# Kernel tuning notes

Measured on AMD Instinct MI355X. Metric: run time of the kernel, lower is better.

The kernel has to match this reference:

```python
import jax, jax.numpy as jnp
import numpy as np

BATCH, DIM = 8192, 1024  # batch of ODE states, state dimension (orig dim=100 scaled up)
ETA = 1.0                # self.eta
B_DECAY = 1.0            # self.B (linear decay coefficient)


def setup_inputs() -> dict:
    key = jax.random.key(0)
    k1, k2, k3, k4, k5 = jax.random.split(key, 5)
    return {
        "x":      jax.random.normal(k1, (BATCH, DIM), jnp.float32),
        "e_x":    jax.random.normal(k2, (BATCH, DIM), jnp.float32),
        "W":      jax.random.normal(k3, (BATCH, DIM), jnp.float32),
        "A":      jax.random.normal(k4, (DIM, DIM), jnpp := jnp.float32) / np.float32(np.sqrt(DIM)),
        "target": jax.random.normal(k5, (1, DIM), jnp.float32),
    }


def reference(x, e_x, W, A, target):
    # b_ast = diagonal of B_ast = diag(target^2 / (1 + target^2)); mm with a diag
    # matrix == elementwise multiply by its diagonal.  [1, D]
    b_ast = target ** 2 / (1.0 + target ** 2)
    # control: u = -eta * (W * (x + e_x - target)) @ B_ast              [B, D]
    u = -ETA * (W * ((x + e_x) - target)) * b_ast
    # saturating nonlinearity sigma(x) = x^2 / (1 + x^2)                [B, D]
    sig = x ** 2 / (1.0 + x ** 2)
    # dx = -B*x + A @ sigma(x) (per state: sigma(x) @ A^T) + u*sigma(x) [B, D]
    dx = -B_DECAY * x + sig @ A.T + u * sig
    # original returns tuple(dx_i) + tuple(-dx_i) + tuple(zeros): stack as [3, B, D]
    return jnp.stack([dx, -dx, jnp.zeros_like(dx)])
```

## Files before the change

kernel.cpp:

```cpp
#include <hip/hip_runtime.h>
#include <hip/hip_bf16.h>
#include <stdint.h>

#define BATCH 8192
#define DIM   1024
#define BM 64
#define BN 64
#define BK 64
#define NT (DIM / BK)

typedef __attribute__((ext_vector_type(4))) float f32x4;
typedef __attribute__((ext_vector_type(8))) short bf16x8;
typedef __attribute__((ext_vector_type(4))) unsigned short u16x4;
typedef __attribute__((ext_vector_type(8))) unsigned short u16x8;

#define AS1(p) ((const __attribute__((address_space(1))) void*)(p))
#define AS3(p) ((__attribute__((address_space(3))) void*)(p))

__device__ __forceinline__ unsigned short f2bf(float f) {
    union { __hip_bfloat16 h; unsigned short u; } v;
    v.h = __hip_bfloat16(f);
    return v.u;
}

__device__ __forceinline__ float sigma_f(float x) {
    float x2 = x * x;
    return x2 * __builtin_amdgcn_rcpf(1.0f + x2);
}

__global__ __launch_bounds__(256) void convA_kernel(
    const float* __restrict__ A, unsigned short* __restrict__ Ab)
{
    int idx = blockIdx.x * 256 + threadIdx.x;
    f32x4 av = ((const f32x4*)A)[idx];
    u16x4 ab;
#pragma unroll
    for (int i = 0; i < 4; ++i) ab[i] = f2bf(av[i]);
    ((u16x4*)Ab)[idx] = ab;
}

__global__ __launch_bounds__(256, 5) void fused_kernel(
    const float* __restrict__ x, const float* __restrict__ ex,
    const float* __restrict__ W, const float* __restrict__ tgt,
    const unsigned short* __restrict__ Ab,
    float* __restrict__ out0, float* __restrict__ out1,
    float* __restrict__ out2)
{
    __shared__ __align__(16) char lds[32768];

    const int b     = blockIdx.x;
    const int xcd   = b & 7;
    const int local = b >> 3;
    const int bm    = xcd * 16 + (local >> 4);
    const int bn    = local & 15;

    const int tid  = threadIdx.x;
    const int lane = tid & 63;
    const int wid  = tid >> 6;
    const int wr   = wid >> 1;
    const int wc   = wid & 1;
    const int l15  = lane & 15;

    const int swz = (((lane & 7) ^ (lane >> 3)) << 4);
    const char* gBb = (const char*)Ab +
        ((size_t)(bn * BN + wid * 16 + (lane >> 3)) * DIM) * 2 + swz;

    const int r0 = tid >> 3;
    const int g  = tid & 7;
    const float* gx = x + (size_t)(bm * BM + r0) * DIM + g * 8;
    const int wAoff = (g * 16) ^ ((r0 & 7) << 4);

    const int rd_sw = (lane & 7) << 4;
    const int cb0   = (lane >> 4) << 4;

    f32x4 acc[2][2];
#pragma unroll
    for (int mi = 0; mi < 2; ++mi)
#pragma unroll
        for (int ni = 0; ni < 2; ++ni)
            acc[mi][ni] = f32x4{0.f, 0.f, 0.f, 0.f};

    auto stageB = [&](int k, char* Bs) {
#pragma unroll
        for (int j = 0; j < 2; ++j)
            __builtin_amdgcn_global_load_lds(
                AS1(gBb + (size_t)j * (8 * DIM * 2) + (size_t)k * 2),
                AS3(Bs + (wid * 16 + j * 8) * 128), 16, 0, 0);
    };
    auto loadX = [&](int k, f32x4 xa[2][2]) {
#pragma unroll
        for (int s = 0; s < 2; ++s) {
            xa[s][0] = *(const f32x4*)(gx + (size_t)s * 32 * DIM + k);
            xa[s][1] = *(const f32x4*)(gx + (size_t)s * 32 * DIM + k + 4);
        }
    };
    auto writeSig = [&](char* As, f32x4 xa[2][2]) {
#pragma unroll
        for (int s = 0; s < 2; ++s) {
            u16x8 sb;
#pragma unroll
            for (int i = 0; i < 4; ++i) {
                sb[i]     = f2bf(sigma_f(xa[s][0][i]));
                sb[i + 4] = f2bf(sigma_f(xa[s][1][i]));
            }
            *(u16x8*)(As + (r0 + s * 32) * 128 + wAoff) = sb;
        }
    };

    {
        f32x4 xa[2][2];
        loadX(0, xa);
        stageB(0, lds + 8192);
        writeSig(lds, xa);
    }
    __syncthreads();

    for (int t = 0; t < NT; ++t) {
        const int cur = t & 1;
        f32x4 xa[2][2];
        if (t + 1 < NT) {
            loadX((t + 1) * BK, xa);
            stageB((t + 1) * BK, lds + (cur ^ 1) * 16384 + 8192);
        }
        __builtin_amdgcn_sched_barrier(0);

        const char* As_ = lds + cur * 16384;
        const char* Bs_ = As_ + 8192;
#pragma unroll
        for (int kk = 0; kk < 2; ++kk) {
            bf16x8 af[2], bfr[2];
#pragma unroll
            for (int mi = 0; mi < 2; ++mi)
                af[mi] = *(const bf16x8*)(As_ + (wr * 32 + mi * 16 + l15) * 128 +
                                          ((cb0 + kk * 64) ^ rd_sw));
#pragma unroll
            for (int ni = 0; ni < 2; ++ni)
                bfr[ni] = *(const bf16x8*)(Bs_ + (wc * 32 + ni * 16 + l15) * 128 +
                                           ((cb0 + kk * 64) ^ rd_sw));
#pragma unroll
            for (int mi = 0; mi < 2; ++mi)
#pragma unroll
                for (int ni = 0; ni < 2; ++ni)
                    acc[mi][ni] = __builtin_amdgcn_mfma_f32_16x16x32_bf16(
                        af[mi], bfr[ni], acc[mi][ni], 0, 0, 0);
        }
        __builtin_amdgcn_sched_barrier(0);

        if (t + 1 < NT) writeSig(lds + (cur ^ 1) * 16384, xa);
        __syncthreads();
    }

#pragma unroll
    for (int mi = 0; mi < 2; ++mi)
#pragma unroll
        for (int ni = 0; ni < 2; ++ni) {
            const int row_ = wr * 32 + mi * 16 + ((lane >> 4) << 2);
            const int colb = (wc * 32 + ni * 16 + l15) * 4;
#pragma unroll
            for (int r = 0; r < 4; ++r)
                *(float*)(lds + (row_ + r) * 256 + colb) = acc[mi][ni][r];
        }
    __syncthreads();

#pragma unroll
    for (int p = 0; p < 4; ++p) {
        const int ci  = tid + p * 256;
        const int row = ci >> 4;
        const int cv  = ci & 15;
        f32x4 c = *(const f32x4*)(lds + row * 256 + cv * 16);
        const size_t v4 = (size_t)(bm * BM + row) * (DIM / 4) + bn * (BN / 4) + cv;
        f32x4 xv = ((const f32x4*)x)[v4];
        f32x4 ev = ((const f32x4*)ex)[v4];
        f32x4 wv = ((const f32x4*)W)[v4];
        f32x4 tv = ((const f32x4*)tgt)[bn * (BN / 4) + cv];
        f32x4 o0;
#pragma unroll
        for (int e = 0; e < 4; ++e) {
            float xi = xv[e], ti = tv[e];
            float ba = ti * ti * __builtin_amdgcn_rcpf(1.0f + ti * ti);
            float u  = -(wv[e] * (xi + ev[e] - ti)) * ba;
            float s  = sigma_f(xi);
            o0[e] = -xi + u * s + c[e];
        }
        ((f32x4*)out0)[v4] = o0;
        ((f32x4*)out1)[v4] = -o0;
        ((f32x4*)out2)[v4] = f32x4{0.f, 0.f, 0.f, 0.f};
    }
}

extern "C" void kernel_launch(void* const* d_in, const int* in_sizes, int n_in,
                              void* d_out, int out_size, void* d_ws, size_t ws_size,
                              hipStream_t stream)
{
    const float* x   = (const float*)d_in[0];
    const float* ex  = (const float*)d_in[1];
    const float* W   = (const float*)d_in[2];
    const float* A   = (const float*)d_in[3];
    const float* tgt = (const float*)d_in[4];

    float* out0 = (float*)d_out;
    float* out1 = out0 + (size_t)BATCH * DIM;
    float* out2 = out1 + (size_t)BATCH * DIM;

    unsigned short* Abf = (unsigned short*)d_ws;

    convA_kernel<<<DIM * DIM / 4 / 256, 256, 0, stream>>>(A, Abf);
    fused_kernel<<<(BATCH / BM) * (DIM / BN), 256, 0, stream>>>(
        x, ex, W, tgt, Abf, out0, out1, out2);
}
```

Baseline: 65.63 us.

## Load GEMM operands directly into registers and enlarge tile to 128x64

The main GEMM loop no longer stages sigma(x) and bf16 A tiles through shared memory. Each wave now loads its own x rows and the B fragments from global memory straight into MFMA operand layout, computes sigma in registers, and double-buffers these register sets without any __syncthreads. The block tile grows to 128x64 with one wave per 32-row strip, and the XCD block mapping is changed. This removes LDS traffic and barriers, but every wave reloads the full B tile, which increases global/L2 traffic, and register pressure rises (launch bounds drop from 5 to 4).

```diff
diff --git a/kernel.cpp b/kernel.cpp
--- a/kernel.cpp
+++ b/kernel.cpp
@@ -4,18 +4,11 @@
 
 #define BATCH 8192
 #define DIM   1024
-#define BM 64
-#define BN 64
-#define BK 64
-#define NT (DIM / BK)
 
 typedef __attribute__((ext_vector_type(4))) float f32x4;
 typedef __attribute__((ext_vector_type(8))) short bf16x8;
 typedef __attribute__((ext_vector_type(4))) unsigned short u16x4;
 typedef __attribute__((ext_vector_type(8))) unsigned short u16x8;
-
-#define AS1(p) ((const __attribute__((address_space(1))) void*)(p))
-#define AS3(p) ((__attribute__((address_space(3))) void*)(p))
 
 __device__ __forceinline__ unsigned short f2bf(float f) {
     union { __hip_bfloat16 h; unsigned short u; } v;
@@ -39,7 +32,7 @@
     ((u16x4*)Ab)[idx] = ab;
 }
 
-__global__ __launch_bounds__(256, 5) void fused_kernel(
+__global__ __launch_bounds__(256, 4) void fused_kernel(
     const float* __restrict__ x, const float* __restrict__ ex,
     const float* __restrict__ W, const float* __restrict__ tgt,
     const unsigned short* __restrict__ Ab,
@@ -48,114 +41,79 @@
 {
     __shared__ __align__(16) char lds[32768];
 
-    const int b     = blockIdx.x;
-    const int xcd   = b & 7;
-    const int local = b >> 3;
-    const int bm    = xcd * 16 + (local >> 4);
-    const int bn    = local & 15;
+    const int b    = blockIdx.x;
+    const int xcd  = b & 7;
+    const int idx  = b >> 3;
+    const int bm   = (idx >> 4) * 8 + xcd;
+    const int bn   = idx & 15;
 
     const int tid  = threadIdx.x;
     const int lane = tid & 63;
     const int wid  = tid >> 6;
-    const int wr   = wid >> 1;
-    const int wc   = wid & 1;
     const int l15  = lane & 15;
+    const int kgo  = (lane >> 4) << 3;
 
-    const int swz = (((lane & 7) ^ (lane >> 3)) << 4);
-    const char* gBb = (const char*)Ab +
-        ((size_t)(bn * BN + wid * 16 + (lane >> 3)) * DIM) * 2 + swz;
+    const float* gxa0 = x + (size_t)(bm * 128 + wid * 32 + l15) * DIM + kgo;
+    const float* gxa1 = gxa0 + (size_t)16 * DIM;
+    const unsigned short* gb0 = Ab + (size_t)(bn * 64 + l15) * DIM + kgo;
 
-    const int r0 = tid >> 3;
-    const int g  = tid & 7;
-    const float* gx = x + (size_t)(bm * BM + r0) * DIM + g * 8;
-    const int wAoff = (g * 16) ^ ((r0 & 7) << 4);
-
-    const int rd_sw = (lane & 7) << 4;
-    const int cb0   = (lane >> 4) << 4;
-
-    f32x4 acc[2][2];
+    f32x4 acc[2][4];
 #pragma unroll
     for (int mi = 0; mi < 2; ++mi)
 #pragma unroll
-        for (int ni = 0; ni < 2; ++ni)
+        for (int ni = 0; ni < 4; ++ni)
             acc[mi][ni] = f32x4{0.f, 0.f, 0.f, 0.f};
 
-    auto stageB = [&](int k, char* Bs) {
+    f32x4 xe[2][2], xo[2][2];
+    bf16x8 be[4], bo[4];
+
+    auto LOADX = [&](int kt, f32x4 xa[2][2]) {
+        xa[0][0] = *(const f32x4*)(gxa0 + kt * 32);
+        xa[0][1] = *(const f32x4*)(gxa0 + kt * 32 + 4);
+        xa[1][0] = *(const f32x4*)(gxa1 + kt * 32);
+        xa[1][1] = *(const f32x4*)(gxa1 + kt * 32 + 4);
+    };
+    auto LOADB = [&](int kt, bf16x8 bf[4]) {
 #pragma unroll
-        for (int j = 0; j < 2; ++j)
-            __builtin_amdgcn_global_load_lds(
-                AS1(gBb + (size_t)j * (8 * DIM * 2) + (size_t)k * 2),
-                AS3(Bs + (wid * 16 + j * 8) * 128), 16, 0, 0);
+        for (int ni = 0; ni < 4; ++ni)
+            bf[ni] = *(const bf16x8*)(gb0 + (size_t)ni * 16 * DIM + kt * 32);
     };
-    auto loadX = [&](int k, f32x4 xa[2][2]) {
+    auto COMPUTE = [&](f32x4 xa[2][2], bf16x8 bf[4]) {
 #pragma unroll
-        for (int s = 0; s < 2; ++s) {
-            xa[s][0] = *(const f32x4*)(gx + (size_t)s * 32 * DIM + k);
-            xa[s][1] = *(const f32x4*)(gx + (size_t)s * 32 * DIM + k + 4);
-        }
-    };
-    auto writeSig = [&](char* As, f32x4 xa[2][2]) {
-#pragma unroll
-        for (int s = 0; s < 2; ++s) {
-            u16x8 sb;
+        for (int mi = 0; mi < 2; ++mi) {
+            union { u16x8 u; bf16x8 b; } cv;
 #pragma unroll
             for (int i = 0; i < 4; ++i) {
-                sb[i]     = f2bf(sigma_f(xa[s][0][i]));
-                sb[i + 4] = f2bf(sigma_f(xa[s][1][i]));
+                cv.u[i]     = f2bf(sigma_f(xa[mi][0][i]));
+                cv.u[i + 4] = f2bf(sigma_f(xa[mi][1][i]));
             }
-            *(u16x8*)(As + (r0 + s * 32) * 128 + wAoff) = sb;
+#pragma unroll
+            for (int ni = 0; ni < 4; ++ni)
+                acc[mi][ni] = __builtin_amdgcn_mfma_f32_16x16x32_bf16(
+                    cv.b, bf[ni], acc[mi][ni], 0, 0, 0);
         }
     };
 
-    {
-        f32x4 xa[2][2];
-        loadX(0, xa);
-        stageB(0, lds + 8192);
-        writeSig(lds, xa);
-    }
-    __syncthreads();
-
-    for (int t = 0; t < NT; ++t) {
-        const int cur = t & 1;
-        f32x4 xa[2][2];
-        if (t + 1 < NT) {
-            loadX((t + 1) * BK, xa);
-            stageB((t + 1) * BK, lds + (cur ^ 1) * 16384 + 8192);
-        }
+    LOADX(0, xe);
+    LOADB(0, be);
+#pragma unroll
+    for (int kt = 0; kt < 32; kt += 2) {
+        if (kt + 1 < 32) { LOADX(kt + 1, xo); LOADB(kt + 1, bo); }
         __builtin_amdgcn_sched_barrier(0);
-
-        const char* As_ = lds + cur * 16384;
-        const char* Bs_ = As_ + 8192;
-#pragma unroll
-        for (int kk = 0; kk < 2; ++kk) {
-            bf16x8 af[2], bfr[2];
-#pragma unroll
-            for (int mi = 0; mi < 2; ++mi)
-                af[mi] = *(const bf16x8*)(As_ + (wr * 32 + mi * 16 + l15) * 128 +
-                                          ((cb0 + kk * 64) ^ rd_sw));
-#pragma unroll
-            for (int ni = 0; ni < 2; ++ni)
-                bfr[ni] = *(const bf16x8*)(Bs_ + (wc * 32 + ni * 16 + l15) * 128 +
-                                           ((cb0 + kk * 64) ^ rd_sw));
-#pragma unroll
-            for (int mi = 0; mi < 2; ++mi)
-#pragma unroll
-                for (int ni = 0; ni < 2; ++ni)
-                    acc[mi][ni] = __builtin_amdgcn_mfma_f32_16x16x32_bf16(
-                        af[mi], bfr[ni], acc[mi][ni], 0, 0, 0);
-        }
+        COMPUTE(xe, be);
         __builtin_amdgcn_sched_barrier(0);
-
-        if (t + 1 < NT) writeSig(lds + (cur ^ 1) * 16384, xa);
-        __syncthreads();
+        if (kt + 2 < 32) { LOADX(kt + 2, xe); LOADB(kt + 2, be); }
+        __builtin_amdgcn_sched_barrier(0);
+        COMPUTE(xo, bo);
+        __builtin_amdgcn_sched_barrier(0);
     }
 
 #pragma unroll
     for (int mi = 0; mi < 2; ++mi)
 #pragma unroll
-        for (int ni = 0; ni < 2; ++ni) {
-            const int row_ = wr * 32 + mi * 16 + ((lane >> 4) << 2);
-            const int colb = (wc * 32 + ni * 16 + l15) * 4;
+        for (int ni = 0; ni < 4; ++ni) {
+            const int row_ = wid * 32 + mi * 16 + ((lane >> 4) << 2);
+            const int colb = (ni * 16 + l15) * 4;
 #pragma unroll
             for (int r = 0; r < 4; ++r)
                 *(float*)(lds + (row_ + r) * 256 + colb) = acc[mi][ni][r];
@@ -163,16 +121,16 @@
     __syncthreads();
 
 #pragma unroll
-    for (int p = 0; p < 4; ++p) {
+    for (int p = 0; p < 8; ++p) {
         const int ci  = tid + p * 256;
         const int row = ci >> 4;
         const int cv  = ci & 15;
         f32x4 c = *(const f32x4*)(lds + row * 256 + cv * 16);
-        const size_t v4 = (size_t)(bm * BM + row) * (DIM / 4) + bn * (BN / 4) + cv;
+        const size_t v4 = (size_t)(bm * 128 + row) * (DIM / 4) + bn * 16 + cv;
         f32x4 xv = ((const f32x4*)x)[v4];
         f32x4 ev = ((const f32x4*)ex)[v4];
         f32x4 wv = ((const f32x4*)W)[v4];
-        f32x4 tv = ((const f32x4*)tgt)[bn * (BN / 4) + cv];
+        f32x4 tv = ((const f32x4*)tgt)[bn * 16 + cv];
         f32x4 o0;
 #pragma unroll
         for (int e = 0; e < 4; ++e) {
@@ -205,6 +163,6 @@
     unsigned short* Abf = (unsigned short*)d_ws;
 
     convA_kernel<<<DIM * DIM / 4 / 256, 256, 0, stream>>>(A, Abf);
-    fused_kernel<<<(BATCH / BM) * (DIM / BN), 256, 0, stream>>>(
+    fused_kernel<<<(BATCH / 128) * (DIM / 64), 256, 0, stream>>>(
         x, ex, W, tgt, Abf, out0, out1, out2);
 }
```

New measurement: 134.5 us. 2.05x slower.

## Persistent two-tile blocks with queued decoupled epilogue via bf16 C workspace

Applied to the files above, without the earlier changes.

Switches to a persistent grid of 512 blocks. Each block computes two 128x64 GEMM tiles and writes each result as bf16 into a global workspace. A global atomic queue then hands finished tiles to any block, which runs the elementwise epilogue, and zero-filling of out2 is spread between the phases. The aim is to overlap the memory-bound epilogue stores with the MFMA work and get larger tile reuse. In exchange it adds a spin-wait queue, an extra bf16 round trip for C that costs precision, and it needs the 512 blocks to be co-resident to avoid deadlock.

```diff
diff --git a/kernel.cpp b/kernel.cpp
--- a/kernel.cpp
+++ b/kernel.cpp
@@ -4,10 +4,11 @@
 
 #define BATCH 8192
 #define DIM   1024
-#define BM 64
+#define BM 128
 #define BN 64
 #define BK 64
-#define NT (DIM / BK)
+#define NT 16
+#define NTILE 1024
 
 typedef __attribute__((ext_vector_type(4))) float f32x4;
 typedef __attribute__((ext_vector_type(8))) short bf16x8;
@@ -22,16 +23,21 @@
     v.h = __hip_bfloat16(f);
     return v.u;
 }
-
+__device__ __forceinline__ float bf2f(unsigned short u) {
+    union { unsigned int i; float f; } v; v.i = (unsigned int)u << 16;
+    return v.f;
+}
 __device__ __forceinline__ float sigma_f(float x) {
     float x2 = x * x;
     return x2 * __builtin_amdgcn_rcpf(1.0f + x2);
 }
 
 __global__ __launch_bounds__(256) void convA_kernel(
-    const float* __restrict__ A, unsigned short* __restrict__ Ab)
+    const float* __restrict__ A, unsigned short* __restrict__ Ab,
+    unsigned* __restrict__ hdr)
 {
     int idx = blockIdx.x * 256 + threadIdx.x;
+    if (idx < 2 + NTILE) hdr[idx] = 0;
     f32x4 av = ((const f32x4*)A)[idx];
     u16x4 ab;
 #pragma unroll
@@ -39,152 +45,213 @@
     ((u16x4*)Ab)[idx] = ab;
 }
 
-__global__ __launch_bounds__(256, 5) void fused_kernel(
+__global__ __launch_bounds__(256, 2) void fused_kernel(
     const float* __restrict__ x, const float* __restrict__ ex,
     const float* __restrict__ W, const float* __restrict__ tgt,
     const unsigned short* __restrict__ Ab,
+    unsigned short* __restrict__ Cws, unsigned* __restrict__ hdr,
     float* __restrict__ out0, float* __restrict__ out1,
     float* __restrict__ out2)
 {
-    __shared__ __align__(16) char lds[32768];
-
-    const int b     = blockIdx.x;
-    const int xcd   = b & 7;
-    const int local = b >> 3;
-    const int bm    = xcd * 16 + (local >> 4);
-    const int bn    = local & 15;
+    __shared__ __align__(16) char lds[81920];
+    __shared__ int shE;
+    char* Cl = lds + 49152;
+
+    const int b   = blockIdx.x;
+    const int bsw = (b & 7) * 64 + (b >> 3);
+    const int T0  = bsw, T1 = bsw + 512;
 
     const int tid  = threadIdx.x;
     const int lane = tid & 63;
     const int wid  = tid >> 6;
-    const int wr   = wid >> 1;
-    const int wc   = wid & 1;
+    const int wr   = wid >> 1, wc = wid & 1;
     const int l15  = lane & 15;
-
-    const int swz = (((lane & 7) ^ (lane >> 3)) << 4);
-    const char* gBb = (const char*)Ab +
-        ((size_t)(bn * BN + wid * 16 + (lane >> 3)) * DIM) * 2 + swz;
-
-    const int r0 = tid >> 3;
-    const int g  = tid & 7;
-    const float* gx = x + (size_t)(bm * BM + r0) * DIM + g * 8;
+    const int swz  = (((lane & 7) ^ (lane >> 3)) << 4);
+    const int r0   = tid >> 3;
+    const int g    = tid & 7;
     const int wAoff = (g * 16) ^ ((r0 & 7) << 4);
-
     const int rd_sw = (lane & 7) << 4;
     const int cb0   = (lane >> 4) << 4;
 
-    f32x4 acc[2][2];
-#pragma unroll
-    for (int mi = 0; mi < 2; ++mi)
-#pragma unroll
-        for (int ni = 0; ni < 2; ++ni)
-            acc[mi][ni] = f32x4{0.f, 0.f, 0.f, 0.f};
-
-    auto stageB = [&](int k, char* Bs) {
-#pragma unroll
-        for (int j = 0; j < 2; ++j)
-            __builtin_amdgcn_global_load_lds(
-                AS1(gBb + (size_t)j * (8 * DIM * 2) + (size_t)k * 2),
-                AS3(Bs + (wid * 16 + j * 8) * 128), 16, 0, 0);
-    };
-    auto loadX = [&](int k, f32x4 xa[2][2]) {
-#pragma unroll
-        for (int s = 0; s < 2; ++s) {
-            xa[s][0] = *(const f32x4*)(gx + (size_t)s * 32 * DIM + k);
-            xa[s][1] = *(const f32x4*)(gx + (size_t)s * 32 * DIM + k + 4);
-        }
-    };
-    auto writeSig = [&](char* As, f32x4 xa[2][2]) {
-#pragma unroll
-        for (int s = 0; s < 2; ++s) {
-            u16x8 sb;
-#pragma unroll
-            for (int i = 0; i < 4; ++i) {
-                sb[i]     = f2bf(sigma_f(xa[s][0][i]));
-                sb[i + 4] = f2bf(sigma_f(xa[s][1][i]));
-            }
-            *(u16x8*)(As + (r0 + s * 32) * 128 + wAoff) = sb;
-        }
-    };
-
-    {
-        f32x4 xa[2][2];
-        loadX(0, xa);
-        stageB(0, lds + 8192);
-        writeSig(lds, xa);
-    }
-    __syncthreads();
-
-    for (int t = 0; t < NT; ++t) {
-        const int cur = t & 1;
-        f32x4 xa[2][2];
-        if (t + 1 < NT) {
-            loadX((t + 1) * BK, xa);
-            stageB((t + 1) * BK, lds + (cur ^ 1) * 16384 + 8192);
-        }
-        __builtin_amdgcn_sched_barrier(0);
-
-        const char* As_ = lds + cur * 16384;
-        const char* Bs_ = As_ + 8192;
-#pragma unroll
-        for (int kk = 0; kk < 2; ++kk) {
-            bf16x8 af[2], bfr[2];
-#pragma unroll
-            for (int mi = 0; mi < 2; ++mi)
-                af[mi] = *(const bf16x8*)(As_ + (wr * 32 + mi * 16 + l15) * 128 +
-                                          ((cb0 + kk * 64) ^ rd_sw));
+    unsigned* q = hdr + 2;
+
+    auto gemmTile = [&](int t) {
+        const int bm = t >> 4, bn = t & 15;
+        const float* gx = x + (size_t)(bm * BM + r0) * DIM + g * 8;
+        const char* gBb = (const char*)Ab +
+            ((size_t)(bn * BN + wid * 8 + (lane >> 3)) * DIM) * 2 + swz;
+
+        f32x4 acc[4][2];
+#pragma unroll
+        for (int mi = 0; mi < 4; ++mi)
 #pragma unroll
             for (int ni = 0; ni < 2; ++ni)
-                bfr[ni] = *(const bf16x8*)(Bs_ + (wc * 32 + ni * 16 + l15) * 128 +
-                                           ((cb0 + kk * 64) ^ rd_sw));
-#pragma unroll
-            for (int mi = 0; mi < 2; ++mi)
+                acc[mi][ni] = f32x4{0.f, 0.f, 0.f, 0.f};
+
+        auto stageB = [&](int k, char* Bs) {
+#pragma unroll
+            for (int j = 0; j < 2; ++j)
+                __builtin_amdgcn_global_load_lds(
+                    AS1(gBb + (size_t)j * (32 * DIM * 2) + (size_t)k * 2),
+                    AS3(Bs + (wid * 8 + j * 32) * 128), 16, 0, 0);
+        };
+        auto loadX = [&](int k, f32x4 xa[4][2]) {
+#pragma unroll
+            for (int s = 0; s < 4; ++s) {
+                xa[s][0] = *(const f32x4*)(gx + (size_t)s * 32 * DIM + k);
+                xa[s][1] = *(const f32x4*)(gx + (size_t)s * 32 * DIM + k + 4);
+            }
+        };
+        auto writeSig = [&](char* As, f32x4 xa[4][2]) {
+#pragma unroll
+            for (int s = 0; s < 4; ++s) {
+                u16x8 sb;
+#pragma unroll
+                for (int i = 0; i < 4; ++i) {
+                    sb[i]     = f2bf(sigma_f(xa[s][0][i]));
+                    sb[i + 4] = f2bf(sigma_f(xa[s][1][i]));
+                }
+                *(u16x8*)(As + (r0 + s * 32) * 128 + wAoff) = sb;
+            }
+        };
+
+        {
+            f32x4 xa[4][2];
+            loadX(0, xa);
+            stageB(0, lds + 16384);
+            writeSig(lds, xa);
+        }
+        __syncthreads();
+
+        for (int it = 0; it < NT; ++it) {
+            const int cur = it & 1;
+            char* bufn = lds + (cur ^ 1) * 24576;
+            f32x4 xa[4][2];
+            if (it + 1 < NT) {
+                loadX((it + 1) * BK, xa);
+                stageB((it + 1) * BK, bufn + 16384);
+            }
+            __builtin_amdgcn_sched_barrier(0);
+            const char* As_ = lds + cur * 24576;
+            const char* Bs_ = As_ + 16384;
+#pragma unroll
+            for (int kk = 0; kk < 2; ++kk) {
+                bf16x8 af[4], bfr[2];
+#pragma unroll
+                for (int mi = 0; mi < 4; ++mi)
+                    af[mi] = *(const bf16x8*)(As_ + (wr * 64 + mi * 16 + l15) * 128 +
+                                              ((cb0 + kk * 64) ^ rd_sw));
 #pragma unroll
                 for (int ni = 0; ni < 2; ++ni)
-                    acc[mi][ni] = __builtin_amdgcn_mfma_f32_16x16x32_bf16(
-                        af[mi], bfr[ni], acc[mi][ni], 0, 0, 0);
-        }
-        __builtin_amdgcn_sched_barrier(0);
-
-        if (t + 1 < NT) writeSig(lds + (cur ^ 1) * 16384, xa);
-        __syncthreads();
-    }
-
-#pragma unroll
-    for (int mi = 0; mi < 2; ++mi)
-#pragma unroll
-        for (int ni = 0; ni < 2; ++ni) {
-            const int row_ = wr * 32 + mi * 16 + ((lane >> 4) << 2);
-            const int colb = (wc * 32 + ni * 16 + l15) * 4;
-#pragma unroll
-            for (int r = 0; r < 4; ++r)
-                *(float*)(lds + (row_ + r) * 256 + colb) = acc[mi][ni][r];
-        }
-    __syncthreads();
-
-#pragma unroll
-    for (int p = 0; p < 4; ++p) {
-        const int ci  = tid + p * 256;
-        const int row = ci >> 4;
-        const int cv  = ci & 15;
-        f32x4 c = *(const f32x4*)(lds + row * 256 + cv * 16);
-        const size_t v4 = (size_t)(bm * BM + row) * (DIM / 4) + bn * (BN / 4) + cv;
-        f32x4 xv = ((const f32x4*)x)[v4];
-        f32x4 ev = ((const f32x4*)ex)[v4];
-        f32x4 wv = ((const f32x4*)W)[v4];
-        f32x4 tv = ((const f32x4*)tgt)[bn * (BN / 4) + cv];
-        f32x4 o0;
-#pragma unroll
-        for (int e = 0; e < 4; ++e) {
-            float xi = xv[e], ti = tv[e];
-            float ba = ti * ti * __builtin_amdgcn_rcpf(1.0f + ti * ti);
-            float u  = -(wv[e] * (xi + ev[e] - ti)) * ba;
-            float s  = sigma_f(xi);
-            o0[e] = -xi + u * s + c[e];
-        }
-        ((f32x4*)out0)[v4] = o0;
-        ((f32x4*)out1)[v4] = -o0;
-        ((f32x4*)out2)[v4] = f32x4{0.f, 0.f, 0.f, 0.f};
+                    bfr[ni] = *(const bf16x8*)(Bs_ + (wc * 32 + ni * 16 + l15) * 128 +
+                                               ((cb0 + kk * 64) ^ rd_sw));
+#pragma unroll
+                for (int mi = 0; mi < 4; ++mi)
+#pragma unroll
+                    for (int ni = 0; ni < 2; ++ni)
+                        acc[mi][ni] = __builtin_amdgcn_mfma_f32_16x16x32_bf16(
+                            af[mi], bfr[ni], acc[mi][ni], 0, 0, 0);
+            }
+            __builtin_amdgcn_sched_barrier(0);
+            if (it + 1 < NT) writeSig(bufn, xa);
+            __syncthreads();
+        }
+
+#pragma unroll
+        for (int mi = 0; mi < 4; ++mi)
+#pragma unroll
+            for (int ni = 0; ni < 2; ++ni) {
+                const int row_ = wr * 64 + mi * 16 + ((lane >> 4) << 2);
+                const int colb = (wc * 32 + ni * 16 + l15) * 4;
+#pragma unroll
+                for (int r = 0; r < 4; ++r)
+                    *(float*)(Cl + (row_ + r) * 256 + colb) = acc[mi][ni][r];
+            }
+        __syncthreads();
+
+        u16x4* Cq = (u16x4*)Cws + (size_t)t * 2048;
+#pragma unroll
+        for (int p = 0; p < 8; ++p) {
+            const int ci = p * 256 + tid, row = ci >> 4, cv = ci & 15;
+            f32x4 c = *(const f32x4*)(Cl + row * 256 + cv * 16);
+            u16x4 cb;
+#pragma unroll
+            for (int e = 0; e < 4; ++e) cb[e] = f2bf(c[e]);
+            Cq[ci] = cb;
+        }
+        __syncthreads();
+    };
+
+    auto pushT = [&](int t) {
+        if (tid == 0) {
+            unsigned slot = atomicAdd(&hdr[0], 1u);
+            __hip_atomic_store(&q[slot], (unsigned)(t + 1),
+                               __ATOMIC_RELEASE, __HIP_MEMORY_SCOPE_AGENT);
+        }
+    };
+
+    auto popEpi = [&]() {
+        if (tid == 0) {
+            unsigned tk = atomicAdd(&hdr[1], 1u);
+            unsigned v;
+            for (;;) {
+                v = __hip_atomic_load(&q[tk], __ATOMIC_RELAXED,
+                                      __HIP_MEMORY_SCOPE_AGENT);
+                if (v) break;
+                __builtin_amdgcn_s_sleep(2);
+            }
+            (void)__hip_atomic_load(&q[tk], __ATOMIC_ACQUIRE,
+                                    __HIP_MEMORY_SCOPE_AGENT);
+            shE = (int)v - 1;
+        }
+        __syncthreads();
+        const int e   = shE;
+        const int ebm = e >> 4, ebn = e & 15;
+        const u16x4* Cq = (const u16x4*)Cws + (size_t)e * 2048;
+#pragma unroll
+        for (int p = 0; p < 8; ++p) {
+            const int ci = p * 256 + tid, row = ci >> 4, cv = ci & 15;
+            u16x4 cb = Cq[ci];
+            const size_t v4 = (size_t)(ebm * BM + row) * (DIM / 4) + ebn * 16 + cv;
+            f32x4 xv = ((const f32x4*)x)[v4];
+            f32x4 evv = ((const f32x4*)ex)[v4];
+            f32x4 wv = ((const f32x4*)W)[v4];
+            f32x4 tv = ((const f32x4*)tgt)[ebn * 16 + cv];
+            f32x4 o0;
+#pragma unroll
+            for (int ee = 0; ee < 4; ++ee) {
+                float xi = xv[ee], ti = tv[ee];
+                float ba = ti * ti * __builtin_amdgcn_rcpf(1.0f + ti * ti);
+                float u  = -(wv[ee] * (xi + evv[ee] - ti)) * ba;
+                float s  = sigma_f(xi);
+                o0[ee] = -xi + u * s + bf2f(cb[ee]);
+            }
+            ((f32x4*)out0)[v4] = o0;
+            ((f32x4*)out1)[v4] = -o0;
+        }
+        __syncthreads();
+    };
+
+    auto zeroT = [&](int t) {
+        const int zbm = t >> 4, zbn = t & 15;
+#pragma unroll
+        for (int p = 0; p < 8; ++p) {
+            const int ci = p * 256 + tid, row = ci >> 4, cv = ci & 15;
+            ((f32x4*)out2)[(size_t)(zbm * BM + row) * (DIM / 4) + zbn * 16 + cv] =
+                f32x4{0.f, 0.f, 0.f, 0.f};
+        }
+    };
+
+    gemmTile(T0); pushT(T0);
+    if (b & 1) {
+        popEpi();
+        zeroT(T0); zeroT(T1);
+        gemmTile(T1); pushT(T1);
+        popEpi();
+    } else {
+        gemmTile(T1); pushT(T1);
+        zeroT(T0); zeroT(T1);
+        popEpi(); popEpi();
     }
 }
 
@@ -203,8 +270,10 @@
     float* out2 = out1 + (size_t)BATCH * DIM;
 
     unsigned short* Abf = (unsigned short*)d_ws;
-
-    convA_kernel<<<DIM * DIM / 4 / 256, 256, 0, stream>>>(A, Abf);
-    fused_kernel<<<(BATCH / BM) * (DIM / BN), 256, 0, stream>>>(
-        x, ex, W, tgt, Abf, out0, out1, out2);
-}
+    unsigned short* Cws = (unsigned short*)((char*)d_ws + (size_t)2 * 1024 * 1024);
+    unsigned*       hdr = (unsigned*)((char*)d_ws + (size_t)18 * 1024 * 1024);
+
+    convA_kernel<<<DIM * DIM / 4 / 256, 256, 0, stream>>>(A, Abf, hdr);
+    fused_kernel<<<512, 256, 0, stream>>>(x, ex, W, tgt, Abf, Cws, hdr,
+                                          out0, out1, out2);
+}
```

Result: slower. 147.4 us (+124.6%).

## Split work into concurrent GEMM and elementwise blocks plus bf16 combine pass

Applied to the files above, without the earlier changes.

The separate A-to-bf16 conversion kernel is removed; A is now converted to bf16 while it is staged into LDS. The first kernel interleaves GEMM blocks (128x64 tiles) with elementwise blocks that compute the bias term and the zero output, so memory-bound and MFMA work can overlap. The GEMM result goes to a bf16 workspace, and a second kernel adds it to out0 and writes out1. The cost is extra round trips: out0 is written and read back, the workspace is written and read, and the GEMM result picks up additional bf16 rounding.

```diff
diff --git a/kernel.cpp b/kernel.cpp
--- a/kernel.cpp
+++ b/kernel.cpp
@@ -4,187 +4,216 @@
 
 #define BATCH 8192
 #define DIM   1024
-#define BM 64
+#define BM 128
 #define BN 64
 #define BK 64
-#define NT (DIM / BK)
+#define NT 16
+#define NV4 (BATCH * DIM / 4)
 
 typedef __attribute__((ext_vector_type(4))) float f32x4;
 typedef __attribute__((ext_vector_type(8))) short bf16x8;
 typedef __attribute__((ext_vector_type(4))) unsigned short u16x4;
 typedef __attribute__((ext_vector_type(8))) unsigned short u16x8;
 
-#define AS1(p) ((const __attribute__((address_space(1))) void*)(p))
-#define AS3(p) ((__attribute__((address_space(3))) void*)(p))
-
 __device__ __forceinline__ unsigned short f2bf(float f) {
     union { __hip_bfloat16 h; unsigned short u; } v;
     v.h = __hip_bfloat16(f);
     return v.u;
 }
-
+__device__ __forceinline__ float bf2f(unsigned short u) {
+    union { unsigned int i; float f; } v; v.i = (unsigned int)u << 16;
+    return v.f;
+}
 __device__ __forceinline__ float sigma_f(float x) {
     float x2 = x * x;
     return x2 * __builtin_amdgcn_rcpf(1.0f + x2);
 }
 
-__global__ __launch_bounds__(256) void convA_kernel(
-    const float* __restrict__ A, unsigned short* __restrict__ Ab)
-{
-    int idx = blockIdx.x * 256 + threadIdx.x;
-    f32x4 av = ((const f32x4*)A)[idx];
-    u16x4 ab;
-#pragma unroll
-    for (int i = 0; i < 4; ++i) ab[i] = f2bf(av[i]);
-    ((u16x4*)Ab)[idx] = ab;
-}
-
-__global__ __launch_bounds__(256, 5) void fused_kernel(
+__global__ __launch_bounds__(256, 3) void k1_kernel(
     const float* __restrict__ x, const float* __restrict__ ex,
     const float* __restrict__ W, const float* __restrict__ tgt,
-    const unsigned short* __restrict__ Ab,
-    float* __restrict__ out0, float* __restrict__ out1,
-    float* __restrict__ out2)
+    const float* __restrict__ A,
+    unsigned short* __restrict__ Cws,
+    float* __restrict__ out0, float* __restrict__ out2)
 {
-    __shared__ __align__(16) char lds[32768];
-
-    const int b     = blockIdx.x;
-    const int xcd   = b & 7;
-    const int local = b >> 3;
-    const int bm    = xcd * 16 + (local >> 4);
-    const int bn    = local & 15;
-
-    const int tid  = threadIdx.x;
-    const int lane = tid & 63;
-    const int wid  = tid >> 6;
-    const int wr   = wid >> 1;
-    const int wc   = wid & 1;
-    const int l15  = lane & 15;
-
-    const int swz = (((lane & 7) ^ (lane >> 3)) << 4);
-    const char* gBb = (const char*)Ab +
-        ((size_t)(bn * BN + wid * 16 + (lane >> 3)) * DIM) * 2 + swz;
-
-    const int r0 = tid >> 3;
-    const int g  = tid & 7;
-    const float* gx = x + (size_t)(bm * BM + r0) * DIM + g * 8;
-    const int wAoff = (g * 16) ^ ((r0 & 7) << 4);
-
-    const int rd_sw = (lane & 7) << 4;
-    const int cb0   = (lane >> 4) << 4;
-
-    f32x4 acc[2][2];
-#pragma unroll
-    for (int mi = 0; mi < 2; ++mi)
-#pragma unroll
-        for (int ni = 0; ni < 2; ++ni)
-            acc[mi][ni] = f32x4{0.f, 0.f, 0.f, 0.f};
-
-    auto stageB = [&](int k, char* Bs) {
-#pragma unroll
-        for (int j = 0; j < 2; ++j)
-            __builtin_amdgcn_global_load_lds(
-                AS1(gBb + (size_t)j * (8 * DIM * 2) + (size_t)k * 2),
-                AS3(Bs + (wid * 16 + j * 8) * 128), 16, 0, 0);
-    };
-    auto loadX = [&](int k, f32x4 xa[2][2]) {
-#pragma unroll
-        for (int s = 0; s < 2; ++s) {
-            xa[s][0] = *(const f32x4*)(gx + (size_t)s * 32 * DIM + k);
-            xa[s][1] = *(const f32x4*)(gx + (size_t)s * 32 * DIM + k + 4);
+    __shared__ __align__(16) char lds[49152];
+
+    const int b = blockIdx.x;
+    const int tid = threadIdx.x;
+
+    if (((b >> 3) & 1) == 0) {
+        const int gt = (b >> 4) * 8 + (b & 7);
+        const int bm = gt >> 4;
+        const int bn = gt & 15;
+
+        const int lane = tid & 63;
+        const int wid  = tid >> 6;
+        const int wr   = wid >> 1, wc = wid & 1;
+        const int l15  = lane & 15;
+        const int r0   = tid >> 3;
+        const int g    = tid & 7;
+        const int wAoff = (g * 16) ^ ((r0 & 7) << 4);
+        const int rd_sw = (lane & 7) << 4;
+        const int cb0   = (lane >> 4) << 4;
+
+        const float* gx = x + (size_t)(bm * BM + r0) * DIM + g * 8;
+        const float* gA = A + (size_t)(bn * BN + r0) * DIM + g * 8;
+
+        f32x4 acc[4][2];
+#pragma unroll
+        for (int mi = 0; mi < 4; ++mi)
+#pragma unroll
+            for (int ni = 0; ni < 2; ++ni)
+                acc[mi][ni] = f32x4{0.f, 0.f, 0.f, 0.f};
+
+        f32x4 xa[4][2], bv[2][2];
+
+        auto loadX = [&](int k) {
+#pragma unroll
+            for (int s = 0; s < 4; ++s) {
+                xa[s][0] = *(const f32x4*)(gx + (size_t)s * 32 * DIM + k);
+                xa[s][1] = *(const f32x4*)(gx + (size_t)s * 32 * DIM + k + 4);
+            }
+        };
+        auto loadB = [&](int k) {
+#pragma unroll
+            for (int s = 0; s < 2; ++s) {
+                bv[s][0] = *(const f32x4*)(gA + (size_t)s * 32 * DIM + k);
+                bv[s][1] = *(const f32x4*)(gA + (size_t)s * 32 * DIM + k + 4);
+            }
+        };
+        auto writeStage = [&](char* buf) {
+            char* As = buf;
+            char* Bs = buf + 16384;
+#pragma unroll
+            for (int s = 0; s < 4; ++s) {
+                u16x8 sb;
+#pragma unroll
+                for (int i = 0; i < 4; ++i) {
+                    sb[i]     = f2bf(sigma_f(xa[s][0][i]));
+                    sb[i + 4] = f2bf(sigma_f(xa[s][1][i]));
+                }
+                *(u16x8*)(As + (r0 + s * 32) * 128 + wAoff) = sb;
+            }
+#pragma unroll
+            for (int s = 0; s < 2; ++s) {
+                u16x8 sb;
+#pragma unroll
+                for (int i = 0; i < 4; ++i) {
+                    sb[i]     = f2bf(bv[s][0][i]);
+                    sb[i + 4] = f2bf(bv[s][1][i]);
+                }
+                *(u16x8*)(Bs + (r0 + s * 32) * 128 + wAoff) = sb;
+            }
+        };
+
+        loadX(0); loadB(0);
+        writeStage(lds);
+        __syncthreads();
+
+        for (int t = 0; t < NT; ++t) {
+            const int cur = t & 1;
+            if (t + 1 < NT) { loadX((t + 1) * BK); loadB((t + 1) * BK); }
+            __builtin_amdgcn_sched_barrier(0);
+
+            const char* As_ = lds + cur * 24576;
+            const char* Bs_ = As_ + 16384;
+#pragma unroll
+            for (int kk = 0; kk < 2; ++kk) {
+                bf16x8 af[4], bfr[2];
+#pragma unroll
+                for (int mi = 0; mi < 4; ++mi)
+                    af[mi] = *(const bf16x8*)(As_ + (wr * 64 + mi * 16 + l15) * 128 +
+                                              ((cb0 + kk * 64) ^ rd_sw));
+#pragma unroll
+                for (int ni = 0; ni < 2; ++ni)
+                    bfr[ni] = *(const bf16x8*)(Bs_ + (wc * 32 + ni * 16 + l15) * 128 +
+                                               ((cb0 + kk * 64) ^ rd_sw));
+#pragma unroll
+                for (int mi = 0; mi < 4; ++mi)
+#pragma unroll
+                    for (int ni = 0; ni < 2; ++ni)
+                        acc[mi][ni] = __builtin_amdgcn_mfma_f32_16x16x32_bf16(
+                            af[mi], bfr[ni], acc[mi][ni], 0, 0, 0);
+            }
+            __builtin_amdgcn_sched_barrier(0);
+            if (t + 1 < NT) writeStage(lds + (cur ^ 1) * 24576);
+            __syncthreads();
         }
-    };
-    auto writeSig = [&](char* As, f32x4 xa[2][2]) {
-#pragma unroll
-        for (int s = 0; s < 2; ++s) {
-            u16x8 sb;
-#pragma unroll
-            for (int i = 0; i < 4; ++i) {
-                sb[i]     = f2bf(sigma_f(xa[s][0][i]));
-                sb[i + 4] = f2bf(sigma_f(xa[s][1][i]));
-            }
-            *(u16x8*)(As + (r0 + s * 32) * 128 + wAoff) = sb;
+
+#pragma unroll
+        for (int mi = 0; mi < 4; ++mi)
+#pragma unroll
+            for (int ni = 0; ni < 2; ++ni) {
+                const int row_ = wr * 64 + mi * 16 + ((lane >> 4) << 2);
+                const int colb = (wc * 32 + ni * 16 + l15) * 4;
+#pragma unroll
+                for (int r = 0; r < 4; ++r)
+                    *(float*)(lds + (row_ + r) * 256 + colb) = acc[mi][ni][r];
+            }
+        __syncthreads();
+
+        unsigned short* Ct = Cws + (size_t)gt * (BM * BN);
+#pragma unroll
+        for (int p = 0; p < 4; ++p) {
+            const int ci  = p * 256 + tid;
+            const int row = ci >> 3;
+            const int gg  = ci & 7;
+            f32x4 c0 = *(const f32x4*)(lds + row * 256 + gg * 32);
+            f32x4 c1 = *(const f32x4*)(lds + row * 256 + gg * 32 + 16);
+            u16x8 cb;
+#pragma unroll
+            for (int e = 0; e < 4; ++e) {
+                cb[e]     = f2bf(c0[e]);
+                cb[e + 4] = f2bf(c1[e]);
+            }
+            *(u16x8*)(Ct + row * BN + gg * 8) = cb;
         }
-    };
-
-    {
-        f32x4 xa[2][2];
-        loadX(0, xa);
-        stageB(0, lds + 8192);
-        writeSig(lds, xa);
+    } else {
+        const int s = (b >> 4) * 8 + (b & 7);
+        const int i0 = s * 256 + tid;
+#pragma unroll
+        for (int p = 0; p < 8; ++p) {
+            const int v4 = i0 + p * 262144;
+            const int cv = v4 & 255;
+            f32x4 xv = ((const f32x4*)x)[v4];
+            f32x4 ev = ((const f32x4*)ex)[v4];
+            f32x4 wv = ((const f32x4*)W)[v4];
+            f32x4 tv = ((const f32x4*)tgt)[cv];
+            f32x4 bq;
+#pragma unroll
+            for (int e = 0; e < 4; ++e) {
+                float xi = xv[e], ti = tv[e];
+                float ba = ti * ti * __builtin_amdgcn_rcpf(1.0f + ti * ti);
+                float u  = -(wv[e] * (xi + ev[e] - ti)) * ba;
+                float sg = sigma_f(xi);
+                bq[e] = -xi + u * sg;
+            }
+            ((f32x4*)out0)[v4] = bq;
+            ((f32x4*)out2)[v4] = f32x4{0.f, 0.f, 0.f, 0.f};
+        }
     }
-    __syncthreads();
-
-    for (int t = 0; t < NT; ++t) {
-        const int cur = t & 1;
-        f32x4 xa[2][2];
-        if (t + 1 < NT) {
-            loadX((t + 1) * BK, xa);
-            stageB((t + 1) * BK, lds + (cur ^ 1) * 16384 + 8192);
-        }
-        __builtin_amdgcn_sched_barrier(0);
-
-        const char* As_ = lds + cur * 16384;
-        const char* Bs_ = As_ + 8192;
-#pragma unroll
-        for (int kk = 0; kk < 2; ++kk) {
-            bf16x8 af[2], bfr[2];
-#pragma unroll
-            for (int mi = 0; mi < 2; ++mi)
-                af[mi] = *(const bf16x8*)(As_ + (wr * 32 + mi * 16 + l15) * 128 +
-                                          ((cb0 + kk * 64) ^ rd_sw));
-#pragma unroll
-            for (int ni = 0; ni < 2; ++ni)
-                bfr[ni] = *(const bf16x8*)(Bs_ + (wc * 32 + ni * 16 + l15) * 128 +
-                                           ((cb0 + kk * 64) ^ rd_sw));
-#pragma unroll
-            for (int mi = 0; mi < 2; ++mi)
-#pragma unroll
-                for (int ni = 0; ni < 2; ++ni)
-                    acc[mi][ni] = __builtin_amdgcn_mfma_f32_16x16x32_bf16(
-                        af[mi], bfr[ni], acc[mi][ni], 0, 0, 0);
-        }
-        __builtin_amdgcn_sched_barrier(0);
-
-        if (t + 1 < NT) writeSig(lds + (cur ^ 1) * 16384, xa);
-        __syncthreads();
-    }
-
-#pragma unroll
-    for (int mi = 0; mi < 2; ++mi)
-#pragma unroll
-        for (int ni = 0; ni < 2; ++ni) {
-            const int row_ = wr * 32 + mi * 16 + ((lane >> 4) << 2);
-            const int colb = (wc * 32 + ni * 16 + l15) * 4;
-#pragma unroll
-            for (int r = 0; r < 4; ++r)
-                *(float*)(lds + (row_ + r) * 256 + colb) = acc[mi][ni][r];
-        }
-    __syncthreads();
-
+}
+
+__global__ __launch_bounds__(256) void k2_kernel(
+    const unsigned short* __restrict__ Cws,
+    float* __restrict__ out0, float* __restrict__ out1)
+{
+    const int i0 = blockIdx.x * 256 + threadIdx.x;
 #pragma unroll
     for (int p = 0; p < 4; ++p) {
-        const int ci  = tid + p * 256;
-        const int row = ci >> 4;
-        const int cv  = ci & 15;
-        f32x4 c = *(const f32x4*)(lds + row * 256 + cv * 16);
-        const size_t v4 = (size_t)(bm * BM + row) * (DIM / 4) + bn * (BN / 4) + cv;
-        f32x4 xv = ((const f32x4*)x)[v4];
-        f32x4 ev = ((const f32x4*)ex)[v4];
-        f32x4 wv = ((const f32x4*)W)[v4];
-        f32x4 tv = ((const f32x4*)tgt)[bn * (BN / 4) + cv];
+        const int v4  = i0 + p * 524288;
+        const int m   = v4 >> 8;
+        const int cv  = v4 & 255;
+        const int gt  = (m >> 7) * 16 + (cv >> 4);
+        const int off = (m & 127) * BN + (cv & 15) * 4;
+        u16x4 cb = *(const u16x4*)(Cws + (size_t)gt * (BM * BN) + off);
+        f32x4 bq = ((const f32x4*)out0)[v4];
         f32x4 o0;
 #pragma unroll
-        for (int e = 0; e < 4; ++e) {
-            float xi = xv[e], ti = tv[e];
-            float ba = ti * ti * __builtin_amdgcn_rcpf(1.0f + ti * ti);
-            float u  = -(wv[e] * (xi + ev[e] - ti)) * ba;
-            float s  = sigma_f(xi);
-            o0[e] = -xi + u * s + c[e];
-        }
+        for (int e = 0; e < 4; ++e) o0[e] = bq[e] + bf2f(cb[e]);
         ((f32x4*)out0)[v4] = o0;
         ((f32x4*)out1)[v4] = -o0;
-        ((f32x4*)out2)[v4] = f32x4{0.f, 0.f, 0.f, 0.f};
     }
 }
 
@@ -202,9 +231,8 @@
     float* out1 = out0 + (size_t)BATCH * DIM;
     float* out2 = out1 + (size_t)BATCH * DIM;
 
-    unsigned short* Abf = (unsigned short*)d_ws;
-
-    convA_kernel<<<DIM * DIM / 4 / 256, 256, 0, stream>>>(A, Abf);
-    fused_kernel<<<(BATCH / BM) * (DIM / BN), 256, 0, stream>>>(
-        x, ex, W, tgt, Abf, out0, out1, out2);
-}
+    unsigned short* Cws = (unsigned short*)d_ws;
+
+    k1_kernel<<<2048, 256, 0, stream>>>(x, ex, W, tgt, A, Cws, out0, out2);
+    k2_kernel<<<2048, 256, 0, stream>>>(Cws, out0, out1);
+}
```

Result: slower. 111.6 us (+70.0%).
